# Kernel optimization log

Hardware: AMD Instinct MI355X
Metric: run time of the kernel (lower is better)

Reference implementation:

```python
import jax, jax.numpy as jnp
import numpy as np

# db4 decomposition low-pass filter, pywt coefficient order
DEC_LO = np.array([-0.010597401784997278, 0.032883011666982945,
                   0.030841381835986965, -0.18703481171888114,
                   -0.02798376941698385, 0.6308807679295904,
                   0.7148465705525415, 0.23037781330885523], dtype=np.float32)
LEVEL = 5
B, C, L = 64, 64, 8192


def _qmf_hi(dec_lo):
    # pywt relation: dec_hi[n] = (-1)^(n+1) * dec_lo[F-1-n]
    F = dec_lo.shape[0]
    signs = jnp.where(jnp.arange(F) % 2 == 0, -1.0, 1.0).astype(dec_lo.dtype)
    return signs * dec_lo[::-1]


def _wavedec(x, dec_lo, dec_hi):
    # pywt.dwt(v, w, 'symmetric') == np.convolve(sym_pad(v, F-1), filt, 'valid')[1::2]
    # implemented as a stride-2 cross-correlation with the reversed filter.
    b, c, n = x.shape
    v = x.reshape(b * c, n)
    F = dec_lo.shape[0]
    # kernel: (out_ch=2 [lo, hi], in_ch=1, width=F); reversed => true convolution
    k = jnp.stack([dec_lo[::-1], dec_hi[::-1]])[:, None, :]
    details = []
    for _ in range(LEVEL):
        ext = jnp.pad(v, ((0, 0), (F - 1, F - 1)), mode='symmetric')[:, 1:]
        y = jax.lax.conv_general_dilated(ext[:, None, :], k,
                                         window_strides=(2,), padding='VALID')
        v = y[:, 0, :]           # approximation -> next level input
        details.append(y[:, 1, :])  # detail for this level (finest first)
    approx = v.reshape(b, c, -1)
    # pywt order: [cA_L, cD_L, ..., cD_1] -> coarsest detail first
    det = [d.reshape(b, c, -1) for d in reversed(details)]
    return (approx, *det)


def setup_inputs() -> dict:
    key = jax.random.key(0)
    x = jax.random.normal(key, (B, C, L), dtype=jnp.float32)
    dec_lo = jnp.asarray(DEC_LO)
    dec_hi = _qmf_hi(dec_lo)
    return {"x": x, "dec_lo": dec_lo, "dec_hi": dec_hi}


def reference(x, dec_lo, dec_hi):
    # Returns (cA_L, cD_L, cD_{L-1}, ..., cD_1), matching the torch module's
    # [approx_tensor, detail_tensors] flattened.
    return _wavedec(x, dec_lo, dec_hi)
```

## Files before the change

kernel.cpp:

```cpp
#include <hip/hip_runtime.h>


static constexpr int ROWS = 64 * 64;
static constexpr int N0 = 8192;
static constexpr int LEN1 = 4099, LEN2 = 2053, LEN3 = 1030, LEN4 = 518, LEN5 = 262;

__global__ __launch_bounds__(256)
void wavedec5_kernel(const float* __restrict__ x,
                     const float* __restrict__ dlo,
                     const float* __restrict__ dhi,
                     float* __restrict__ out)
{
    __shared__ __align__(16) float bufA[N0];
    __shared__ __align__(16) float bufB[LEN1 + 1];

    const int row = blockIdx.x;
    const int tid = threadIdx.x;

    float h[8], g[8];
#pragma unroll
    for (int i = 0; i < 8; ++i) { h[i] = dlo[i]; g[i] = dhi[i]; }

    {
        const float4* __restrict__ xin =
            reinterpret_cast<const float4*>(x) + (size_t)row * (N0 / 4);
        float4* bA4 = reinterpret_cast<float4*>(bufA);
#pragma unroll
        for (int i = 0; i < (N0 / 4) / 256; ++i)
            bA4[tid + i * 256] = xin[tid + i * 256];
    }
    __syncthreads();

    const int lens[6] = {N0, LEN1, LEN2, LEN3, LEN4, LEN5};
    const size_t detoff[5] = {16896000u,
                              8486912u,
                              4268032u,
                              2146304u,
                              1073152u};
    float* __restrict__ aout = out + (size_t)row * LEN5;

    float* src = bufA;
    float* dst = bufB;

#pragma unroll
    for (int lvl = 0; lvl < 5; ++lvl) {
        const int n = lens[lvl];
        const int m = lens[lvl + 1];
        float* __restrict__ dout = out + detoff[lvl] + (size_t)row * m;
        for (int pos = tid; pos < m; pos += 256) {
            const int s0 = 2 * pos + 1;
            float a = 0.f, d = 0.f;
#pragma unroll
            for (int q = 0; q < 8; ++q) {
                int s = s0 - q;
                int idx = (s < 0) ? (-1 - s) : ((s >= n) ? (2 * n - 1 - s) : s);
                const float v = src[idx];
                a = fmaf(h[q], v, a);
                d = fmaf(g[q], v, d);
            }
            dout[pos] = d;
            if (lvl == 4) aout[pos] = a;
            else         dst[pos]  = a;
        }
        __syncthreads();
        float* t = src; src = dst; dst = t;
    }
}

extern "C" void kernel_launch(void* const* d_in, const int* in_sizes, int n_in,
                              void* d_out, int out_size, void* d_ws, size_t ws_size,
                              hipStream_t stream) {
    const float* x   = (const float*)d_in[0];
    const float* dlo = (const float*)d_in[1];
    const float* dhi = (const float*)d_in[2];
    float* out = (float*)d_out;
    wavedec5_kernel<<<ROWS, 256, 0, stream>>>(x, dlo, dhi, out);
}
```

Before: 70.55 us.

## Compute first DWT level directly from global memory and shrink LDS footprint

Level 1 now reads the input row straight from global memory instead of staging all 8192 samples in shared memory first. LDS drops from about 48KB to about 24.6KB per block, and the launch bound now asks for 6 blocks per SIMD/CU. Interior positions use four aligned float2 loads with no symmetric-index arithmetic, and only the boundary positions take the old branchy path. The trade-off is that level 1 issues overlapping 32-byte global reads per thread, whose coalescing and cache behaviour differ from the old float4 staging load.

```diff
diff --git a/kernel.cpp b/kernel.cpp
--- a/kernel.cpp
+++ b/kernel.cpp
@@ -1,18 +1,56 @@
 #include <hip/hip_runtime.h>
 
 
-static constexpr int ROWS = 64 * 64;
+static constexpr int ROWS = 4096;
 static constexpr int N0 = 8192;
-static constexpr int LEN1 = 4099, LEN2 = 2053, LEN3 = 1030, LEN4 = 518, LEN5 = 262;
+static constexpr int L1n = 4099, L2n = 2053, L3n = 1030, L4n = 518, L5n = 262;
+static constexpr size_t OFF_D5 = 1073152u;
+static constexpr size_t OFF_D4 = 2146304u;
+static constexpr size_t OFF_D3 = 4268032u;
+static constexpr size_t OFF_D2 = 8486912u;
+static constexpr size_t OFF_D1 = 16896000u;
 
-__global__ __launch_bounds__(256)
+__device__ __forceinline__ void dwt_level(
+    const float* __restrict__ src, int n, int m,
+    const float* __restrict__ h, const float* __restrict__ g,
+    float* __restrict__ adst, float* __restrict__ ddst, int tid)
+{
+    for (int pos = tid; pos < m; pos += 256) {
+        float a = 0.f, d = 0.f;
+        if (pos >= 3 && 2 * pos + 1 < n) {
+            const float2* s2 = reinterpret_cast<const float2*>(src) + (pos - 3);
+            float2 w0 = s2[0], w1 = s2[1], w2 = s2[2], w3 = s2[3];
+            a = fmaf(h[7], w0.x, a); d = fmaf(g[7], w0.x, d);
+            a = fmaf(h[6], w0.y, a); d = fmaf(g[6], w0.y, d);
+            a = fmaf(h[5], w1.x, a); d = fmaf(g[5], w1.x, d);
+            a = fmaf(h[4], w1.y, a); d = fmaf(g[4], w1.y, d);
+            a = fmaf(h[3], w2.x, a); d = fmaf(g[3], w2.x, d);
+            a = fmaf(h[2], w2.y, a); d = fmaf(g[2], w2.y, d);
+            a = fmaf(h[1], w3.x, a); d = fmaf(g[1], w3.x, d);
+            a = fmaf(h[0], w3.y, a); d = fmaf(g[0], w3.y, d);
+        } else {
+            const int s0 = 2 * pos + 1;
+#pragma unroll
+            for (int q = 0; q < 8; ++q) {
+                int s = s0 - q;
+                int idx = (s < 0) ? (-1 - s) : ((s >= n) ? (2 * n - 1 - s) : s);
+                const float v = src[idx];
+                a = fmaf(h[q], v, a);
+                d = fmaf(g[q], v, d);
+            }
+        }
+        ddst[pos] = d;
+        adst[pos] = a;
+    }
+}
+
+__global__ __launch_bounds__(256, 6)
 void wavedec5_kernel(const float* __restrict__ x,
                      const float* __restrict__ dlo,
                      const float* __restrict__ dhi,
                      float* __restrict__ out)
 {
-    __shared__ __align__(16) float bufA[N0];
-    __shared__ __align__(16) float bufB[LEN1 + 1];
+    __shared__ __align__(16) float lds[L1n + 1 + L2n];
 
     const int row = blockIdx.x;
     const int tid = threadIdx.x;
@@ -21,50 +59,18 @@
 #pragma unroll
     for (int i = 0; i < 8; ++i) { h[i] = dlo[i]; g[i] = dhi[i]; }
 
-    {
-        const float4* __restrict__ xin =
-            reinterpret_cast<const float4*>(x) + (size_t)row * (N0 / 4);
-        float4* bA4 = reinterpret_cast<float4*>(bufA);
-#pragma unroll
-        for (int i = 0; i < (N0 / 4) / 256; ++i)
-            bA4[tid + i * 256] = xin[tid + i * 256];
-    }
+    const float* __restrict__ xr = x + (size_t)row * N0;
+
+    dwt_level(xr, N0, L1n, h, g, lds, out + OFF_D1 + (size_t)row * L1n, tid);
     __syncthreads();
-
-    const int lens[6] = {N0, LEN1, LEN2, LEN3, LEN4, LEN5};
-    const size_t detoff[5] = {16896000u,
-                              8486912u,
-                              4268032u,
-                              2146304u,
-                              1073152u};
-    float* __restrict__ aout = out + (size_t)row * LEN5;
-
-    float* src = bufA;
-    float* dst = bufB;
-
-#pragma unroll
-    for (int lvl = 0; lvl < 5; ++lvl) {
-        const int n = lens[lvl];
-        const int m = lens[lvl + 1];
-        float* __restrict__ dout = out + detoff[lvl] + (size_t)row * m;
-        for (int pos = tid; pos < m; pos += 256) {
-            const int s0 = 2 * pos + 1;
-            float a = 0.f, d = 0.f;
-#pragma unroll
-            for (int q = 0; q < 8; ++q) {
-                int s = s0 - q;
-                int idx = (s < 0) ? (-1 - s) : ((s >= n) ? (2 * n - 1 - s) : s);
-                const float v = src[idx];
-                a = fmaf(h[q], v, a);
-                d = fmaf(g[q], v, d);
-            }
-            dout[pos] = d;
-            if (lvl == 4) aout[pos] = a;
-            else         dst[pos]  = a;
-        }
-        __syncthreads();
-        float* t = src; src = dst; dst = t;
-    }
+    dwt_level(lds, L1n, L2n, h, g, lds + 4100, out + OFF_D2 + (size_t)row * L2n, tid);
+    __syncthreads();
+    dwt_level(lds + 4100, L2n, L3n, h, g, lds, out + OFF_D3 + (size_t)row * L3n, tid);
+    __syncthreads();
+    dwt_level(lds, L3n, L4n, h, g, lds + 4100, out + OFF_D4 + (size_t)row * L4n, tid);
+    __syncthreads();
+    dwt_level(lds + 4100, L4n, L5n, h, g,
+              out + (size_t)row * L5n, out + OFF_D5 + (size_t)row * L5n, tid);
 }
 
 extern "C" void kernel_launch(void* const* d_in, const int* in_sizes, int n_in,
```

Measured after the change: 62.25 us. 11.8% less time.
